# Optimization experiments

Measured on AMD Instinct MI355X. Metric: run time of the kernel, lower is better.

Reference implementation:

```python
import jax, jax.numpy as jnp
import numpy as np

N = 100000   # nodes
R = 8        # relations
E = 150000   # edges per relation
D_IN = 128
D_OUT = 128
B = 2        # num_bases


def setup_inputs() -> dict:
    key = jax.random.key(0)
    ks = jax.random.split(key, 7)
    return {
        "x": jax.random.normal(ks[0], (N, D_IN), dtype=jnp.float32),
        "src": jax.random.randint(ks[1], (R, E), 0, N, dtype=jnp.int32),
        "dst": jax.random.randint(ks[2], (R, E), 0, N, dtype=jnp.int32),
        "basis_coeff": jax.random.normal(ks[3], (R, B), dtype=jnp.float32),
        "bases": jax.random.normal(ks[4], (B, D_IN, D_OUT), dtype=jnp.float32) * 0.05,
        "loop_weight": jax.random.normal(ks[5], (D_IN, D_OUT), dtype=jnp.float32) * 0.05,
        "h_bias": jax.random.normal(ks[6], (D_OUT,), dtype=jnp.float32) * 0.01,
    }


def reference(x, src, dst, basis_coeff, bases, loop_weight, h_bias):
    n = x.shape[0]
    # basis-decomposed per-relation weights: [R, D_IN, D_OUT]
    weight = jnp.einsum('rb,bio->rio', basis_coeff, bases)
    # gather src features per relation: [R, E, D_IN]
    msgs = x[src]
    # scatter-add onto dst nodes per relation (SpMM aggregate): [R, N, D_IN]
    agg = jax.vmap(lambda m, d: jax.ops.segment_sum(m, d, num_segments=n))(msgs, dst)
    # right normalization: divide by in-degree (clamped to 1), as in DGL GraphConv norm='right'
    ones = jnp.ones(src.shape[1], dtype=x.dtype)
    deg = jax.vmap(lambda d: jax.ops.segment_sum(ones, d, num_segments=n))(dst)
    agg = agg / jnp.clip(deg, 1.0)[..., None]
    # per-relation weight then sum across relations (HeteroGraphConv 'sum' agg)
    h = jnp.einsum('rni,rio->no', agg, weight)
    # self-loop + bias + activation (dropout = 0.0, eval)
    h = h + x @ loop_weight + h_bias
    return jax.nn.relu(h)
```

## Files before the change

### kernel.cpp

```cpp
#include <hip/hip_runtime.h>
#include <hip/hip_fp16.h>


#define DFEAT 128
#define NREL 8
#define ALDA 264
#define ECAP 1024

typedef __attribute__((ext_vector_type(8))) short bf16x8;
typedef __attribute__((ext_vector_type(4))) float f32x4;
typedef __attribute__((ext_vector_type(2))) float f32x2;

__device__ __forceinline__ ushort f2bf(float f) {
    unsigned u = __float_as_uint(f);
    u += 0x7FFF + ((u >> 16) & 1);
    return (ushort)(u >> 16);
}
__device__ __forceinline__ float bflo(unsigned u) { return __uint_as_float(u << 16); }
__device__ __forceinline__ float bfhi(unsigned u) { return __uint_as_float(u & 0xFFFF0000u); }
__device__ __forceinline__ unsigned pack2bf(float lo, float hi) {
    return (unsigned)f2bf(lo) | ((unsigned)f2bf(hi) << 16);
}

__global__ void fused_pre(const int* __restrict__ dst, int* __restrict__ deg,
                          ushort* __restrict__ rank,
                          const float* __restrict__ x, ushort* __restrict__ xb,
                          const float* __restrict__ bases, const float* __restrict__ loopw,
                          ushort* __restrict__ w2T,
                          int RE, int E, int N, int n4) {
    const int stride = gridDim.x * blockDim.x;
    const int t0 = blockIdx.x * blockDim.x + threadIdx.x;
    for (int i = t0; i < RE; i += stride) {
        int r = i / E;
        int d = dst[i];
        rank[i] = (ushort)atomicAdd(&deg[r * N + d], 1);
    }
    for (int i = t0; i < n4; i += stride) {
        float4 v = ((const float4*)x)[i];
        ushort4 o;
        o.x = f2bf(v.x); o.y = f2bf(v.y); o.z = f2bf(v.z); o.w = f2bf(v.w);
        ((ushort4*)xb)[i] = o;
    }
    for (int i = t0; i < 128 * 384; i += stride) {
        int j = i / 384, k = i % 384;
        float v = (k < 256) ? bases[(k >> 7) * DFEAT * DFEAT + (k & 127) * DFEAT + j]
                            : loopw[(k - 256) * DFEAT + j];
        w2T[i] = f2bf(v);
    }
}

__global__ void scan_block_sums(const int* __restrict__ deg, int* __restrict__ cnt,
                                int* __restrict__ bsums, int N) {
    __shared__ int sdata[256];
    int b = blockIdx.x, t = threadIdx.x;
    int idx = b * 256 + t;
    int sum = 0;
    if (idx < N) {
        #pragma unroll
        for (int r = 0; r < NREL; ++r) sum += deg[r * N + idx];
        cnt[idx] = sum;
    }
    sdata[t] = sum; __syncthreads();
    for (int s = 128; s > 0; s >>= 1) {
        if (t < s) sdata[t] += sdata[t + s];
        __syncthreads();
    }
    if (t == 0) bsums[b] = sdata[0];
}

__global__ void scan_mid(int* __restrict__ bsums, int nb) {
    __shared__ int s[256];
    int t = threadIdx.x;
    int base = t * 4;
    int v[4]; int sum = 0;
    #pragma unroll
    for (int i = 0; i < 4; ++i) {
        v[i] = sum;
        int c = (base + i < nb) ? bsums[base + i] : 0;
        sum += c;
    }
    s[t] = sum; __syncthreads();
    for (int off = 1; off < 256; off <<= 1) {
        int add = (t >= off) ? s[t - off] : 0;
        __syncthreads();
        s[t] += add;
        __syncthreads();
    }
    int excl = (t == 0) ? 0 : s[t - 1];
    #pragma unroll
    for (int i = 0; i < 4; ++i)
        if (base + i < nb) bsums[base + i] = excl + v[i];
}

__global__ void scan_write(const int* __restrict__ cnt, const int* __restrict__ bsums,
                           const int* __restrict__ deg,
                           int* __restrict__ rowStart, unsigned* __restrict__ packed,
                           int N) {
    __shared__ int tsum[256];
    int b = blockIdx.x, t = threadIdx.x;
    int idx = b * 256 + t;
    int c = (idx < N) ? cnt[idx] : 0;
    tsum[t] = c; __syncthreads();
    for (int off = 1; off < 256; off <<= 1) {
        int x = 0;
        if (t >= off) x = tsum[t - off];
        __syncthreads();
        if (t >= off) tsum[t] += x;
        __syncthreads();
    }
    int excl = (t == 0) ? 0 : tsum[t - 1];
    if (idx < N) {
        int rs = bsums[b] + excl;
        rowStart[idx] = rs;
        int pre = 0;
        #pragma unroll
        for (int r = 0; r < NREL; ++r) {
            int dv = deg[r * N + idx];
            packed[r * N + idx] = ((unsigned)(rs + pre) << 11) | (unsigned)dv;
            pre += dv;
        }
    }
}

__global__ void fill_kernel(const int* __restrict__ src, const int* __restrict__ dst,
                            const float* __restrict__ coeff,
                            const ushort* __restrict__ rank,
                            const unsigned* __restrict__ packed,
                            uint2* __restrict__ recs, int RE, int E, int N) {
    int idx = blockIdx.x * blockDim.x + threadIdx.x;
    if (idx >= RE) return;
    int r = idx / E;
    int d = dst[idx];
    unsigned p = packed[r * N + d];
    int pos = (int)(p >> 11) + (int)rank[idx];
    float inv = 1.0f / (float)(p & 2047u);
    __half2 hc = __floats2half2_rn(coeff[2 * r] * inv, coeff[2 * r + 1] * inv);
    uint2 rec;
    rec.x = (unsigned)src[idx];
    rec.y = *(unsigned*)&hc;
    recs[pos] = rec;
}

__global__ __launch_bounds__(256, 5) void gather_gemm(
    const uint2* __restrict__ recs, const int* __restrict__ rowStart,
    const ushort* __restrict__ xb,
    const ushort* __restrict__ w2T, const float* __restrict__ bias,
    float* __restrict__ out, int N, int RE) {
    __shared__ __align__(16) ushort agg[32 * ALDA];
    __shared__ __align__(16) uint2 recsL[ECAP];
    __shared__ int rsl[33];
    const int tid = threadIdx.x;
    const int wave = tid >> 6, lane = tid & 63;
    const int row0 = blockIdx.x * 32;

    if (tid < 33) {
        int d = row0 + tid;
        rsl[tid] = (d < N) ? rowStart[d] : RE;
    }
    __syncthreads();
    const int e0 = rsl[0];
    const int cntE = rsl[32] - e0;
    const bool fits = (cntE <= ECAP);
    {
        const int lim = fits ? cntE : 0;
        for (int k = tid; k < lim; k += 256)
            recsL[k] = recs[e0 + k];
    }
    __syncthreads();

    {
        const int qw = tid >> 4;
        const int h  = tid & 15;

        auto gatherNode = [&](int i, auto getRec) {
            const int s   = rsl[i] - e0;
            const int len = rsl[i + 1] - rsl[i];
            f32x2 A0 = {0.f,0.f}, A1 = {0.f,0.f}, A2 = {0.f,0.f}, A3 = {0.f,0.f};
            f32x2 B0 = {0.f,0.f}, B1 = {0.f,0.f}, B2 = {0.f,0.f}, B3 = {0.f,0.f};
            if (len > 0) {
                const int last = s + len - 1;
                for (int k = 0; k < len; k += 8) {
                    uint2 rc[8];
                    #pragma unroll
                    for (int j = 0; j < 8; ++j) {
                        int li = s + k + j;
                        rc[j] = getRec(li <= last ? li : last);
                    }
                    uint4 u[8];
                    #pragma unroll
                    for (int j = 0; j < 8; ++j)
                        u[j] = *(const uint4*)(xb + (size_t)rc[j].x * DFEAT + h * 8);
                    #pragma unroll
                    for (int j = 0; j < 8; ++j) {
                        bool v = (k + j) < len;
                        __half2 hc = *(__half2*)&rc[j].y;
                        float c0 = v ? __low2float(hc) : 0.f;
                        float c1 = v ? __high2float(hc) : 0.f;
                        f32x2 cc0 = {c0, c0}, cc1 = {c1, c1};
                        uint4 uu = u[j];
                        f32x2 f01 = {bflo(uu.x), bfhi(uu.x)};
                        f32x2 f23 = {bflo(uu.y), bfhi(uu.y)};
                        f32x2 f45 = {bflo(uu.z), bfhi(uu.z)};
                        f32x2 f67 = {bflo(uu.w), bfhi(uu.w)};
                        A0 += cc0 * f01; A1 += cc0 * f23; A2 += cc0 * f45; A3 += cc0 * f67;
                        B0 += cc1 * f01; B1 += cc1 * f23; B2 += cc1 * f45; B3 += cc1 * f67;
                    }
                }
            }
            uint4 w0, w1;
            w0.x = pack2bf(A0.x, A0.y); w0.y = pack2bf(A1.x, A1.y);
            w0.z = pack2bf(A2.x, A2.y); w0.w = pack2bf(A3.x, A3.y);
            w1.x = pack2bf(B0.x, B0.y); w1.y = pack2bf(B1.x, B1.y);
            w1.z = pack2bf(B2.x, B2.y); w1.w = pack2bf(B3.x, B3.y);
            *(uint4*)(agg + i * ALDA + h * 8)       = w0;
            *(uint4*)(agg + i * ALDA + 128 + h * 8) = w1;
        };

        if (fits) {
            #pragma unroll
            for (int p = 0; p < 2; ++p)
                gatherNode(qw + p * 16, [&](int li) { return recsL[li]; });
        } else {
            #pragma unroll
            for (int p = 0; p < 2; ++p)
                gatherNode(qw + p * 16, [&](int li) { return recs[e0 + li]; });
        }
    }
    __syncthreads();

    const int quad = lane >> 4, l16 = lane & 15;
    int arow[2];
    #pragma unroll
    for (int m = 0; m < 2; ++m) {
        int r = row0 + m * 16 + l16;
        arow[m] = (r < N) ? r : 0;
    }

    f32x4 zero = {0.f, 0.f, 0.f, 0.f};
    f32x4 acc[2][2] = {{zero, zero}, {zero, zero}};

    #pragma unroll
    for (int kt = 0; kt < 3; ++kt) {
        bf16x8 bq[4][2];
        #pragma unroll
        for (int t = 0; t < 4; ++t)
            #pragma unroll
            for (int g = 0; g < 2; ++g)
                bq[t][g] = *(const bf16x8*)(w2T + (size_t)(wave * 32 + g * 16 + l16) * 384
                                            + kt * 128 + t * 32 + quad * 8);
        #pragma unroll
        for (int m = 0; m < 2; ++m) {
            #pragma unroll
            for (int t = 0; t < 4; ++t) {
                bf16x8 a;
                if (kt < 2)
                    a = *(const bf16x8*)(agg + (m * 16 + l16) * ALDA + kt * 128 + t * 32 + quad * 8);
                else
                    a = *(const bf16x8*)(xb + (size_t)arow[m] * DFEAT + t * 32 + quad * 8);
                acc[m][0] = __builtin_amdgcn_mfma_f32_16x16x32_bf16(a, bq[t][0], acc[m][0], 0, 0, 0);
                acc[m][1] = __builtin_amdgcn_mfma_f32_16x16x32_bf16(a, bq[t][1], acc[m][1], 0, 0, 0);
            }
        }
    }

    #pragma unroll
    for (int g = 0; g < 2; ++g) {
        int c = wave * 32 + g * 16 + l16;
        float bv = bias[c];
        #pragma unroll
        for (int m = 0; m < 2; ++m) {
            #pragma unroll
            for (int reg = 0; reg < 4; ++reg) {
                int grow = row0 + m * 16 + quad * 4 + reg;
                if (grow < N)
                    out[(size_t)grow * DFEAT + c] = fmaxf(acc[m][g][reg] + bv, 0.f);
            }
        }
    }
}

extern "C" void kernel_launch(void* const* d_in, const int* in_sizes, int n_in,
                              void* d_out, int out_size, void* d_ws, size_t ws_size,
                              hipStream_t stream) {
    const float* x     = (const float*)d_in[0];
    const int*   src   = (const int*)  d_in[1];
    const int*   dst   = (const int*)  d_in[2];
    const float* coeff = (const float*)d_in[3];
    const float* bases = (const float*)d_in[4];
    const float* loopw = (const float*)d_in[5];
    const float* bias  = (const float*)d_in[6];
    float* out = (float*)d_out;

    const int N  = in_sizes[0] / DFEAT;
    const int RE = in_sizes[1];
    const int B  = in_sizes[4] / (DFEAT * DFEAT);
    const int R  = in_sizes[3] / B;
    const int E  = RE / R;
    const int NB = (N + 255) / 256;

    char* ws = (char*)d_ws;
    size_t off = 0;
    auto alloc = [&](size_t bytes) { void* p = ws + off; off = (off + bytes + 255) & ~(size_t)255; return p; };
    int*      deg      = (int*)     alloc((size_t)R * N * sizeof(int));
    ushort*   rank     = (ushort*)  alloc((size_t)RE * sizeof(ushort));
    unsigned* packed   = (unsigned*)alloc((size_t)R * N * sizeof(unsigned));
    int*      cnt      = (int*)     alloc((size_t)N * sizeof(int));
    int*      rowStart = (int*)     alloc((size_t)N * sizeof(int));
    int*      bsums    = (int*)     alloc((size_t)NB * sizeof(int));
    ushort*   w2T      = (ushort*)  alloc((size_t)128 * 384 * sizeof(ushort));
    ushort*   xb       = (ushort*)  alloc((size_t)N * DFEAT * sizeof(ushort));
    uint2*    recs     = (uint2*)   alloc((size_t)RE * sizeof(uint2));

    hipMemsetAsync(deg, 0, (size_t)R * N * sizeof(int), stream);
    fused_pre<<<4096, 256, 0, stream>>>(dst, deg, rank, x, xb, bases, loopw, w2T,
                                        RE, E, N, N * 32);
    scan_block_sums<<<NB, 256, 0, stream>>>(deg, cnt, bsums, N);
    scan_mid<<<1, 256, 0, stream>>>(bsums, NB);
    scan_write<<<NB, 256, 0, stream>>>(cnt, bsums, deg, rowStart, packed, N);
    fill_kernel<<<(RE + 255) / 256, 256, 0, stream>>>(src, dst, coeff, rank, packed,
                                                      recs, RE, E, N);

    gather_gemm<<<(N + 31) / 32, 256, 0, stream>>>(recs, rowStart, xb, w2T,
                                                   bias, out, N, RE);
}
```

Baseline: 285.8 us.

## Replace three-pass scan with decoupled-lookback single pass and atomic cursor fill

Merges the three scan kernels into one single-pass scan that uses a ticket counter and decoupled lookback over per-block status words. It drops the rank and packed arrays: the fill kernel now claims slots with an atomic cursor per destination node and reads degree directly. Launch bounds for the gather GEMM are raised to 6 waves per unit. The intent is fewer launches and less memory traffic. The cost is more atomics in the fill kernel, a nondeterministic edge order within each row, and edges of different relations now interleaved inside a row, which the GEMM must tolerate.

Result: slower. 322.3 us (+12.8%).

```diff
diff --git a/kernel.cpp b/kernel.cpp
--- a/kernel.cpp
+++ b/kernel.cpp
@@ -23,7 +23,6 @@
 }
 
 __global__ void fused_pre(const int* __restrict__ dst, int* __restrict__ deg,
-                          ushort* __restrict__ rank,
                           const float* __restrict__ x, ushort* __restrict__ xb,
                           const float* __restrict__ bases, const float* __restrict__ loopw,
                           ushort* __restrict__ w2T,
@@ -33,7 +32,7 @@
     for (int i = t0; i < RE; i += stride) {
         int r = i / E;
         int d = dst[i];
-        rank[i] = (ushort)atomicAdd(&deg[r * N + d], 1);
+        atomicAdd(&deg[r * N + d], 1);
     }
     for (int i = t0; i < n4; i += stride) {
         float4 v = ((const float4*)x)[i];
@@ -49,57 +48,24 @@
     }
 }
 
-__global__ void scan_block_sums(const int* __restrict__ deg, int* __restrict__ cnt,
-                                int* __restrict__ bsums, int N) {
-    __shared__ int sdata[256];
-    int b = blockIdx.x, t = threadIdx.x;
-    int idx = b * 256 + t;
-    int sum = 0;
+__global__ void scan_onepass(const int* __restrict__ deg,
+                             int* __restrict__ rowStart, int* __restrict__ cursor,
+                             unsigned* __restrict__ status, int* __restrict__ ticket,
+                             int N) {
+    __shared__ int tsum[256];
+    __shared__ int sbid;
+    __shared__ int sbase;
+    const int t = threadIdx.x;
+    if (t == 0) sbid = atomicAdd(ticket, 1);
+    __syncthreads();
+    const int b = sbid;
+    const int idx = b * 256 + t;
+
+    int c = 0;
     if (idx < N) {
         #pragma unroll
-        for (int r = 0; r < NREL; ++r) sum += deg[r * N + idx];
-        cnt[idx] = sum;
-    }
-    sdata[t] = sum; __syncthreads();
-    for (int s = 128; s > 0; s >>= 1) {
-        if (t < s) sdata[t] += sdata[t + s];
-        __syncthreads();
-    }
-    if (t == 0) bsums[b] = sdata[0];
-}
-
-__global__ void scan_mid(int* __restrict__ bsums, int nb) {
-    __shared__ int s[256];
-    int t = threadIdx.x;
-    int base = t * 4;
-    int v[4]; int sum = 0;
-    #pragma unroll
-    for (int i = 0; i < 4; ++i) {
-        v[i] = sum;
-        int c = (base + i < nb) ? bsums[base + i] : 0;
-        sum += c;
-    }
-    s[t] = sum; __syncthreads();
-    for (int off = 1; off < 256; off <<= 1) {
-        int add = (t >= off) ? s[t - off] : 0;
-        __syncthreads();
-        s[t] += add;
-        __syncthreads();
-    }
-    int excl = (t == 0) ? 0 : s[t - 1];
-    #pragma unroll
-    for (int i = 0; i < 4; ++i)
-        if (base + i < nb) bsums[base + i] = excl + v[i];
-}
-
-__global__ void scan_write(const int* __restrict__ cnt, const int* __restrict__ bsums,
-                           const int* __restrict__ deg,
-                           int* __restrict__ rowStart, unsigned* __restrict__ packed,
-                           int N) {
-    __shared__ int tsum[256];
-    int b = blockIdx.x, t = threadIdx.x;
-    int idx = b * 256 + t;
-    int c = (idx < N) ? cnt[idx] : 0;
+        for (int r = 0; r < NREL; ++r) c += deg[r * N + idx];
+    }
     tsum[t] = c; __syncthreads();
     for (int off = 1; off < 256; off <<= 1) {
         int x = 0;
@@ -108,32 +74,40 @@
         if (t >= off) tsum[t] += x;
         __syncthreads();
     }
-    int excl = (t == 0) ? 0 : tsum[t - 1];
+    const int lexcl = tsum[t] - c;
+    const int total = tsum[255];
+
+    if (t == 0) {
+        atomicExch(&status[b], ((unsigned)total << 2) | 1u);
+        int base = 0;
+        for (int p = b - 1; p >= 0; --p) {
+            unsigned s;
+            do { s = atomicOr(&status[p], 0u); } while ((s & 3u) == 0u);
+            base += (int)(s >> 2);
+            if ((s & 3u) == 2u) break;
+        }
+        atomicExch(&status[b], ((unsigned)(base + total) << 2) | 2u);
+        sbase = base;
+    }
+    __syncthreads();
     if (idx < N) {
-        int rs = bsums[b] + excl;
+        int rs = sbase + lexcl;
         rowStart[idx] = rs;
-        int pre = 0;
-        #pragma unroll
-        for (int r = 0; r < NREL; ++r) {
-            int dv = deg[r * N + idx];
-            packed[r * N + idx] = ((unsigned)(rs + pre) << 11) | (unsigned)dv;
-            pre += dv;
-        }
+        cursor[idx]   = rs;
     }
 }
 
 __global__ void fill_kernel(const int* __restrict__ src, const int* __restrict__ dst,
                             const float* __restrict__ coeff,
-                            const ushort* __restrict__ rank,
-                            const unsigned* __restrict__ packed,
+                            const int* __restrict__ deg, int* __restrict__ cursor,
                             uint2* __restrict__ recs, int RE, int E, int N) {
     int idx = blockIdx.x * blockDim.x + threadIdx.x;
     if (idx >= RE) return;
     int r = idx / E;
     int d = dst[idx];
-    unsigned p = packed[r * N + d];
-    int pos = (int)(p >> 11) + (int)rank[idx];
-    float inv = 1.0f / (float)(p & 2047u);
+    int dv = deg[r * N + d];
+    float inv = 1.0f / (float)dv;
+    int pos = atomicAdd(&cursor[d], 1);
     __half2 hc = __floats2half2_rn(coeff[2 * r] * inv, coeff[2 * r + 1] * inv);
     uint2 rec;
     rec.x = (unsigned)src[idx];
@@ -141,7 +115,7 @@
     recs[pos] = rec;
 }
 
-__global__ __launch_bounds__(256, 5) void gather_gemm(
+__global__ __launch_bounds__(256, 6) void gather_gemm(
     const uint2* __restrict__ recs, const int* __restrict__ rowStart,
     const ushort* __restrict__ xb,
     const ushort* __restrict__ w2T, const float* __restrict__ bias,
@@ -302,24 +276,21 @@
     size_t off = 0;
     auto alloc = [&](size_t bytes) { void* p = ws + off; off = (off + bytes + 255) & ~(size_t)255; return p; };
     int*      deg      = (int*)     alloc((size_t)R * N * sizeof(int));
-    ushort*   rank     = (ushort*)  alloc((size_t)RE * sizeof(ushort));
-    unsigned* packed   = (unsigned*)alloc((size_t)R * N * sizeof(unsigned));
-    int*      cnt      = (int*)     alloc((size_t)N * sizeof(int));
+    unsigned* status   = (unsigned*)alloc((size_t)NB * sizeof(unsigned));
+    int*      ticket   = (int*)     alloc(sizeof(int));
+    size_t zeroBytes   = off;
     int*      rowStart = (int*)     alloc((size_t)N * sizeof(int));
-    int*      bsums    = (int*)     alloc((size_t)NB * sizeof(int));
+    int*      cursor   = (int*)     alloc((size_t)N * sizeof(int));
     ushort*   w2T      = (ushort*)  alloc((size_t)128 * 384 * sizeof(ushort));
     ushort*   xb       = (ushort*)  alloc((size_t)N * DFEAT * sizeof(ushort));
     uint2*    recs     = (uint2*)   alloc((size_t)RE * sizeof(uint2));
 
-    hipMemsetAsync(deg, 0, (size_t)R * N * sizeof(int), stream);
-    fused_pre<<<4096, 256, 0, stream>>>(dst, deg, rank, x, xb, bases, loopw, w2T,
+    hipMemsetAsync(deg, 0, zeroBytes, stream);
+    fused_pre<<<4096, 256, 0, stream>>>(dst, deg, x, xb, bases, loopw, w2T,
                                         RE, E, N, N * 32);
-    scan_block_sums<<<NB, 256, 0, stream>>>(deg, cnt, bsums, N);
-    scan_mid<<<1, 256, 0, stream>>>(bsums, NB);
-    scan_write<<<NB, 256, 0, stream>>>(cnt, bsums, deg, rowStart, packed, N);
-    fill_kernel<<<(RE + 255) / 256, 256, 0, stream>>>(src, dst, coeff, rank, packed,
+    scan_onepass<<<NB, 256, 0, stream>>>(deg, rowStart, cursor, status, ticket, N);
+    fill_kernel<<<(RE + 255) / 256, 256, 0, stream>>>(src, dst, coeff, deg, cursor,
                                                       recs, RE, E, N);
-
     gather_gemm<<<(N + 31) / 32, 256, 0, stream>>>(recs, rowStart, xb, w2T,
                                                    bias, out, N, RE);
 }
```

## Merge preprocessing kernels into one cooperative kernel with grid syncs

Applied to the files above, without the earlier changes.

The memset, the degree and rank pass, the conversions, the three scan kernels and the fill kernel are replaced by a single cooperative kernel of 512 blocks that uses grid.sync between phases. This removes several kernel launches and their gaps between dependent phases. The block-offset scan now recomputes each block's prefix by summing the preceding bsums (O(NB) work per block) instead of running a separate mid scan. A fallback to the old launch sequence remains if the cooperative launch fails. The fixed grid of 512 blocks may leave the atomic and conversion phases with less parallelism than the previous 4096-block launch.

Measured after the change: 519.8 us. 81.9% more time.

```diff
diff --git a/kernel.cpp b/kernel.cpp
--- a/kernel.cpp
+++ b/kernel.cpp
@@ -1,5 +1,8 @@
 #include <hip/hip_runtime.h>
 #include <hip/hip_fp16.h>
+#include <hip/hip_cooperative_groups.h>
+
+namespace cg = cooperative_groups;
 
 
 #define DFEAT 128
@@ -20,6 +23,111 @@
 __device__ __forceinline__ float bfhi(unsigned u) { return __uint_as_float(u & 0xFFFF0000u); }
 __device__ __forceinline__ unsigned pack2bf(float lo, float hi) {
     return (unsigned)f2bf(lo) | ((unsigned)f2bf(hi) << 16);
+}
+
+__global__ __launch_bounds__(256, 2) void pre_all(
+    const int* __restrict__ dst, const int* __restrict__ src,
+    const float* __restrict__ coeff, const float* __restrict__ x,
+    const float* __restrict__ bases, const float* __restrict__ loopw,
+    int* __restrict__ deg, ushort* __restrict__ rank,
+    unsigned* __restrict__ packed, int* __restrict__ rowStart,
+    int* __restrict__ cnt, int* __restrict__ bsums,
+    ushort* __restrict__ xb, ushort* __restrict__ w2T,
+    uint2* __restrict__ recs,
+    int RE, int E, int N, int n4, int NB) {
+    cg::grid_group grid = cg::this_grid();
+    __shared__ int sdata[256];
+    const int tid = threadIdx.x;
+    const int gstride = gridDim.x * blockDim.x;
+    const int gt = blockIdx.x * blockDim.x + tid;
+
+    for (int i = gt; i < NREL * N; i += gstride) deg[i] = 0;
+    grid.sync();
+
+    for (int i = gt; i < RE; i += gstride) {
+        int r = i / E;
+        int d = dst[i];
+        rank[i] = (ushort)atomicAdd(&deg[r * N + d], 1);
+    }
+    for (int i = gt; i < n4; i += gstride) {
+        float4 v = ((const float4*)x)[i];
+        ushort4 o;
+        o.x = f2bf(v.x); o.y = f2bf(v.y); o.z = f2bf(v.z); o.w = f2bf(v.w);
+        ((ushort4*)xb)[i] = o;
+    }
+    for (int i = gt; i < 128 * 384; i += gstride) {
+        int j = i / 384, k = i % 384;
+        float v = (k < 256) ? bases[(k >> 7) * DFEAT * DFEAT + (k & 127) * DFEAT + j]
+                            : loopw[(k - 256) * DFEAT + j];
+        w2T[i] = f2bf(v);
+    }
+    grid.sync();
+
+    for (int b = blockIdx.x; b < NB; b += gridDim.x) {
+        int idx = b * 256 + tid;
+        int sum = 0;
+        if (idx < N) {
+            #pragma unroll
+            for (int r = 0; r < NREL; ++r) sum += deg[r * N + idx];
+            cnt[idx] = sum;
+        }
+        sdata[tid] = sum; __syncthreads();
+        for (int s = 128; s > 0; s >>= 1) {
+            if (tid < s) sdata[tid] += sdata[tid + s];
+            __syncthreads();
+        }
+        if (tid == 0) bsums[b] = sdata[0];
+        __syncthreads();
+    }
+    grid.sync();
+
+    for (int b = blockIdx.x; b < NB; b += gridDim.x) {
+        int part = 0;
+        for (int k = tid; k < b; k += 256) part += bsums[k];
+        sdata[tid] = part; __syncthreads();
+        for (int s = 128; s > 0; s >>= 1) {
+            if (tid < s) sdata[tid] += sdata[tid + s];
+            __syncthreads();
+        }
+        const int boff = sdata[0];
+        __syncthreads();
+        int idx = b * 256 + tid;
+        int c = (idx < N) ? cnt[idx] : 0;
+        sdata[tid] = c; __syncthreads();
+        for (int off = 1; off < 256; off <<= 1) {
+            int add = (tid >= off) ? sdata[tid - off] : 0;
+            __syncthreads();
+            sdata[tid] += add;
+            __syncthreads();
+        }
+        const int excl = sdata[tid] - c;
+        if (idx < N) {
+            int rs = boff + excl;
+            rowStart[idx] = rs;
+            int pre = 0;
+            #pragma unroll
+            for (int r = 0; r < NREL; ++r) {
+                int dv = deg[r * N + idx];
+                packed[r * N + idx] = ((unsigned)(rs + pre) << 11) | (unsigned)dv;
+                pre += dv;
+            }
+        }
+        __syncthreads();
+    }
+    grid.sync();
+
+    for (int i = gt; i < RE; i += gstride) {
+        int r = i / E;
+        int d = dst[i];
+        unsigned p = packed[r * N + d];
+        int pos = (int)(p >> 11) + (int)rank[i];
+        float inv = 1.0f / (float)(p & 2047u);
+        __half2 hc = __floats2half2_rn(coeff[2 * r] * inv, coeff[2 * r + 1] * inv);
+        uint2 rec;
+        rec.x = (unsigned)src[i];
+        rec.y = *(unsigned*)&hc;
+        recs[pos] = rec;
+    }
 }
 
 __global__ void fused_pre(const int* __restrict__ dst, int* __restrict__ deg,
@@ -297,6 +405,7 @@
     const int R  = in_sizes[3] / B;
     const int E  = RE / R;
     const int NB = (N + 255) / 256;
+    const int n4 = N * 32;
 
     char* ws = (char*)d_ws;
     size_t off = 0;
@@ -311,14 +420,28 @@
     ushort*   xb       = (ushort*)  alloc((size_t)N * DFEAT * sizeof(ushort));
     uint2*    recs     = (uint2*)   alloc((size_t)RE * sizeof(uint2));
 
-    hipMemsetAsync(deg, 0, (size_t)R * N * sizeof(int), stream);
-    fused_pre<<<4096, 256, 0, stream>>>(dst, deg, rank, x, xb, bases, loopw, w2T,
-                                        RE, E, N, N * 32);
-    scan_block_sums<<<NB, 256, 0, stream>>>(deg, cnt, bsums, N);
-    scan_mid<<<1, 256, 0, stream>>>(bsums, NB);
-    scan_write<<<NB, 256, 0, stream>>>(cnt, bsums, deg, rowStart, packed, N);
-    fill_kernel<<<(RE + 255) / 256, 256, 0, stream>>>(src, dst, coeff, rank, packed,
-                                                      recs, RE, E, N);
+    {
+        void* args[] = {
+            (void*)&dst, (void*)&src, (void*)&coeff, (void*)&x,
+            (void*)&bases, (void*)&loopw,
+            (void*)&deg, (void*)&rank, (void*)&packed, (void*)&rowStart,
+            (void*)&cnt, (void*)&bsums, (void*)&xb, (void*)&w2T, (void*)&recs,
+            (void*)&RE, (void*)&E, (void*)&N, (void*)&n4, (void*)&NB
+        };
+        hipError_t err = hipLaunchCooperativeKernel(
+            (const void*)pre_all, dim3(512), dim3(256), args, 0, stream);
+        if (err != hipSuccess) {
+            (void)hipGetLastError();
+            hipMemsetAsync(deg, 0, (size_t)R * N * sizeof(int), stream);
+            fused_pre<<<4096, 256, 0, stream>>>(dst, deg, rank, x, xb, bases,
+                                                loopw, w2T, RE, E, N, n4);
+            scan_block_sums<<<NB, 256, 0, stream>>>(deg, cnt, bsums, N);
+            scan_mid<<<1, 256, 0, stream>>>(bsums, NB);
+            scan_write<<<NB, 256, 0, stream>>>(cnt, bsums, deg, rowStart, packed, N);
+            fill_kernel<<<(RE + 255) / 256, 256, 0, stream>>>(src, dst, coeff, rank,
+                                                              packed, recs, RE, E, N);
+        }
+    }
 
     gather_gemm<<<(N + 31) / 32, 256, 0, stream>>>(recs, rowStart, xb, w2T,
                                                    bias, out, N, RE);
```
